# Optimization experiments

Measured on AMD Instinct MI355X. Metric: run time of the kernel, lower is better.

Reference implementation:

```python
import jax, jax.numpy as jnp
import numpy as np

BATCH_SIZE = 4096          # B; representation has 2B rows
TEMPERATURE = 0.5


def setup_inputs() -> dict:
    key = jax.random.key(0)
    k1, k2, k3 = jax.random.split(key, 3)
    representation = jax.random.normal(k1, (2 * BATCH_SIZE, 128), dtype=jnp.float32)
    xrecon = jax.random.normal(k2, (2 * BATCH_SIZE, 512), dtype=jnp.float32)
    xorig = jax.random.normal(k3, (2 * BATCH_SIZE, 512), dtype=jnp.float32)
    return {"representation": representation, "xrecon": xrecon, "xorig": xorig}


def _xneg_loss(representation, batch_size, temperature):
    # Cosine similarity matrix [2B, 2B]
    n = representation / (jnp.linalg.norm(representation, axis=-1, keepdims=True) + 1e-8)
    sim = n @ n.T  # [2B, 2B]
    sim = sim / temperature
    two_b = 2 * batch_size
    # Positives: diag(sim, +B) then diag(sim, -B) -> [2B]
    l_pos = jnp.diagonal(sim, offset=batch_size)
    r_pos = jnp.diagonal(sim, offset=-batch_size)
    positives = jnp.concatenate([l_pos, r_pos])  # [2B]
    # NT-Xent: logits row i = [pos_i] + (row i minus diag and minus pos entry).
    # The union of {pos_i} and negatives_i is row i with only the main diagonal
    # removed, so CE with label 0 equals: -pos_i + logsumexp(row_i \ {diag}).
    neg_inf = jnp.finfo(sim.dtype).min
    eye = jnp.eye(two_b, dtype=bool)
    sim_no_diag = jnp.where(eye, neg_inf, sim)
    lse = jax.nn.logsumexp(sim_no_diag, axis=1)  # [2B]
    loss_sum = jnp.sum(lse - positives)           # CrossEntropyLoss(reduction='sum')
    return loss_sum / two_b


def reference(representation, xrecon, xorig):
    # reconstruction=True -> MSELoss (mean reduction)
    recon_loss = jnp.mean((xrecon - xorig) ** 2)
    loss = recon_loss
    # contrastive_loss=True
    closs = _xneg_loss(representation, BATCH_SIZE, TEMPERATURE)
    loss = loss + closs
    # distance_loss=True: MSE between the two halves of representation
    zi, zj = representation[:BATCH_SIZE], representation[BATCH_SIZE:]
    zrecon_loss = jnp.mean((zi - zj) ** 2)
    loss = loss + zrecon_loss
    return (loss, closs, recon_loss, zrecon_loss)
```

## Files before the change

kernel.cpp:

```cpp
#include <hip/hip_runtime.h>
#include <math.h>

#define BATCH 4096
#define NROWS (2 * BATCH)
#define D 128
#define DX 512

constexpr int NSPLIT = 8;
constexpr int NT = 8;
constexpr int SLOTS = NSPLIT * 2;

#define SCALE 1.698644f

#define WS_PART   0
#define WS_RECONP 131072
#define WS_ZRECP  (WS_RECONP + 512)
#define WS_POSP   (WS_ZRECP + 256)
#define WS_LSEP   (WS_POSP + 256)
#define WS_NBFT   (WS_LSEP + 64)

typedef __bf16 bf16x8 __attribute__((ext_vector_type(8)));
typedef __bf16 bf16x2 __attribute__((ext_vector_type(2)));
typedef float  f32x16 __attribute__((ext_vector_type(16)));

__device__ __forceinline__ float wave_reduce(float v) {
    #pragma unroll
    for (int o = 32; o > 0; o >>= 1) v += __shfl_xor(v, o);
    return v;
}

__global__ __launch_bounds__(256) void k_prep(const float* __restrict__ rep,
                                              float* __restrict__ ws) {
    const int w = threadIdx.x >> 6, l = threadIdx.x & 63;
    const int wg = blockIdx.x * 4 + w;
    __bf16* nbfT = (__bf16*)(ws + WS_NBFT);
    const int chunk = l >> 2, el = (l & 3) * 2;
    float zacc = 0.f, pacc = 0.f;
    #pragma unroll
    for (int p = 0; p < 4; ++p) {
        const int i = wg + p * 1024;
        float2 a = *reinterpret_cast<const float2*>(rep + i * D + l * 2);
        float2 b = *reinterpret_cast<const float2*>(rep + (i + BATCH) * D + l * 2);
        float dx = a.x - b.x, dy = a.y - b.y;
        float sa  = wave_reduce(a.x * a.x + a.y * a.y);
        float sb  = wave_reduce(b.x * b.x + b.y * b.y);
        float sab = wave_reduce(a.x * b.x + a.y * b.y);
        float sd  = wave_reduce(dx * dx + dy * dy);
        float ia = 1.0f / (sqrtf(sa) + 1e-8f);
        float ib = 1.0f / (sqrtf(sb) + 1e-8f);
        zacc += sd;
        pacc += sab * ia * ib;
        bf16x2 pa, pb;
        pa.x = (__bf16)(a.x * ia * SCALE); pa.y = (__bf16)(a.y * ia * SCALE);
        pb.x = (__bf16)(b.x * ib * SCALE); pb.y = (__bf16)(b.y * ib * SCALE);
        *reinterpret_cast<bf16x2*>(nbfT + ((size_t)chunk * NROWS + i) * 8 + el) = pa;
        *reinterpret_cast<bf16x2*>(
            nbfT + ((size_t)chunk * NROWS + i + BATCH) * 8 + el) = pb;
    }
    __shared__ float shz[4], shp[4];
    if (l == 0) { shz[w] = zacc; shp[w] = pacc; }
    __syncthreads();
    if (threadIdx.x == 0) {
        ws[WS_ZRECP + blockIdx.x] = shz[0] + shz[1] + shz[2] + shz[3];
        ws[WS_POSP + blockIdx.x] = 4.0f * (shp[0] + shp[1] + shp[2] + shp[3]);
    }
}

__global__ __launch_bounds__(256, 2) void k_lse(const float4* __restrict__ xr,
                                                const float4* __restrict__ xo,
                                                float* __restrict__ ws) {
    const __bf16* __restrict__ nbfT = (const __bf16*)(ws + WS_NBFT);
    const int tid = threadIdx.x;
    const int w = tid >> 6, l = tid & 63;
    const int wr = w >> 1, wc = w & 1;
    const int rblk = blockIdx.x;
    const int split = blockIdx.y;
    const int R0 = rblk * 128;
    const int fid = rblk + 64 * split;

    bf16x8 afrag[2][8];
    #pragma unroll
    for (int rb = 0; rb < 2; ++rb) {
        const int lr = R0 + wr * 64 + rb * 32 + (l & 31);
        #pragma unroll
        for (int s = 0; s < 8; ++s) {
            const int c = 2 * s + (l >> 5);
            afrag[rb][s] = *reinterpret_cast<const bf16x8*>(
                nbfT + ((size_t)c * NROWS + lr) * 8);
        }
    }

    float sumexp[2][16] = {};
    float racc = 0.f;

    for (int t = 0; t < NT; ++t) {
        const int C0 = split * (NT * 128) + t * 128;

        const int ridx = fid * 2048 + t * 256 + tid;
        float4 ra = xr[ridx], rbv = xo[ridx];

        f32x16 acc[2][2] = {};
        #pragma unroll
        for (int s = 0; s < 8; ++s) {
            const int c = 2 * s + (l >> 5);
            const __bf16* base = nbfT + (size_t)c * NROWS * 8;
            const int lc = C0 + wc * 64 + (l & 31);
            bf16x8 b0 = *reinterpret_cast<const bf16x8*>(base + (size_t)lc * 8);
            bf16x8 b1 = *reinterpret_cast<const bf16x8*>(base + (size_t)(lc + 32) * 8);
            acc[0][0] = __builtin_amdgcn_mfma_f32_32x32x16_bf16(
                afrag[0][s], b0, acc[0][0], 0, 0, 0);
            acc[0][1] = __builtin_amdgcn_mfma_f32_32x32x16_bf16(
                afrag[0][s], b1, acc[0][1], 0, 0, 0);
            acc[1][0] = __builtin_amdgcn_mfma_f32_32x32x16_bf16(
                afrag[1][s], b0, acc[1][0], 0, 0, 0);
            acc[1][1] = __builtin_amdgcn_mfma_f32_32x32x16_bf16(
                afrag[1][s], b1, acc[1][1], 0, 0, 0);
        }

        const bool diagt = (C0 == R0);
        #pragma unroll
        for (int rb = 0; rb < 2; ++rb) {
            #pragma unroll
            for (int cb = 0; cb < 2; ++cb) {
                const bool dmask = diagt && (2 * wr + rb) == (2 * wc + cb);
                #pragma unroll
                for (int r = 0; r < 16; ++r) {
                    float e = __builtin_amdgcn_exp2f(acc[rb][cb][r]);
                    if (dmask) {
                        const int rrow = (r & 3) + 8 * (r >> 2) + 4 * (l >> 5);
                        if (rrow == (l & 31)) e = 0.0f;
                    }
                    sumexp[rb][r] += e;
                }
            }
        }

        {
            float dx = ra.x - rbv.x, dy = ra.y - rbv.y;
            float dz = ra.z - rbv.z, dw2 = ra.w - rbv.w;
            racc += dx * dx + dy * dy + dz * dz + dw2 * dw2;
        }
    }

    #pragma unroll
    for (int rb = 0; rb < 2; ++rb) {
        #pragma unroll
        for (int r = 0; r < 16; ++r) {
            float v = sumexp[rb][r];
            #pragma unroll
            for (int m = 1; m <= 16; m <<= 1) v += __shfl_xor(v, m);
            sumexp[rb][r] = v;
        }
    }
    if ((l & 31) == 0) {
        #pragma unroll
        for (int rb = 0; rb < 2; ++rb) {
            #pragma unroll
            for (int r = 0; r < 16; ++r) {
                const int row = R0 + wr * 64 + rb * 32
                              + (r & 3) + 8 * (r >> 2) + 4 * (l >> 5);
                ws[WS_PART + row * SLOTS + split * 2 + wc] = sumexp[rb][r];
            }
        }
    }

    racc = wave_reduce(racc);
    __shared__ float shr[4];
    if (l == 0) shr[w] = racc;
    __syncthreads();
    if (tid == 0) ws[WS_RECONP + fid] = shr[0] + shr[1] + shr[2] + shr[3];
}

__global__ __launch_bounds__(256) void k_rowlse(float* __restrict__ ws) {
    const int q = blockIdx.x, tid = threadIdx.x;
    const int j = tid & 127, h = tid >> 7;
    const int row = q * 128 + j;
    float s = 0.f;
    #pragma unroll
    for (int ss = 0; ss < SLOTS / 2; ++ss)
        s += ws[WS_PART + row * SLOTS + 2 * ss + h];
    __shared__ float red[128];
    if (h) red[j] = s;
    __syncthreads();
    float lg = 0.f;
    if (!h) lg = logf(s + red[j]);
    lg = wave_reduce(lg);
    __shared__ float sh[4];
    const int w = tid >> 6, l = tid & 63;
    if (l == 0) sh[w] = lg;
    __syncthreads();
    if (tid == 0) ws[WS_LSEP + q] = sh[0] + sh[1] + sh[2] + sh[3];
}

__global__ __launch_bounds__(256) void k_combine(const float* __restrict__ ws,
                                                 float* __restrict__ out) {
    const int tid = threadIdx.x;
    float lacc = (tid < 64) ? ws[WS_LSEP + tid] : 0.f;
    float racc = ws[WS_RECONP + tid] + ws[WS_RECONP + 256 + tid];
    float zacc = ws[WS_ZRECP + tid];
    float pacc = ws[WS_POSP + tid];

    lacc = wave_reduce(lacc);
    racc = wave_reduce(racc);
    zacc = wave_reduce(zacc);
    pacc = wave_reduce(pacc);

    __shared__ float sh[4][4];
    const int w = tid >> 6, l = tid & 63;
    if (l == 0) { sh[0][w] = lacc; sh[1][w] = racc; sh[2][w] = zacc; sh[3][w] = pacc; }
    __syncthreads();
    if (tid == 0) {
        float lse = sh[0][0] + sh[0][1] + sh[0][2] + sh[0][3];
        float rec = (sh[1][0] + sh[1][1] + sh[1][2] + sh[1][3]) / (float)(NROWS * DX);
        float zre = (sh[2][0] + sh[2][1] + sh[2][2] + sh[2][3]) / (float)(BATCH * D);
        float pos = sh[3][0] + sh[3][1] + sh[3][2] + sh[3][3];
        float closs = (lse - pos) / (float)NROWS;
        out[0] = rec + closs + zre;
        out[1] = closs;
        out[2] = rec;
        out[3] = zre;
    }
}

extern "C" void kernel_launch(void* const* d_in, const int* in_sizes, int n_in,
                              void* d_out, int out_size, void* d_ws, size_t ws_size,
                              hipStream_t stream) {
    const float* rep = (const float*)d_in[0];
    const float4* xr = (const float4*)d_in[1];
    const float4* xo = (const float4*)d_in[2];
    float* out = (float*)d_out;
    float* ws = (float*)d_ws;

    k_prep<<<256, 256, 0, stream>>>(rep, ws);
    dim3 grid(64, NSPLIT);
    k_lse<<<grid, 256, 0, stream>>>(xr, xo, ws);
    k_rowlse<<<64, 256, 0, stream>>>(ws);
    k_combine<<<1, 256, 0, stream>>>(ws, out);
}
```

Measured before the change: 41.71 us.

## Switch similarity GEMM to FP8 MFMA, double column splits, prefetch recon loads

The normalized representation is now stored as FP8 (e4m3) instead of bf16, and the similarity tiles are computed with fp8×fp8 32x32x16 MFMA. This halves operand bytes loaded per tile. The column dimension is split 16 ways with 4 tiles each instead of 8×8, doubling the grid to improve CU coverage. The MSE reconstruction loads are software-prefetched one iteration ahead, and workspace offsets and the combine kernel are adjusted for the extra partial slots. The risk is reduced accuracy of the logsumexp from FP8 quantization of the cosine-similarity inputs.

```diff
diff --git a/kernel.cpp b/kernel.cpp
--- a/kernel.cpp
+++ b/kernel.cpp
@@ -6,22 +6,23 @@
 #define D 128
 #define DX 512
 
-constexpr int NSPLIT = 8;
-constexpr int NT = 8;
+constexpr int NSPLIT = 16;
+constexpr int NT = 4;
 constexpr int SLOTS = NSPLIT * 2;
 
 #define SCALE 1.698644f
 
 #define WS_PART   0
-#define WS_RECONP 131072
-#define WS_ZRECP  (WS_RECONP + 512)
+#define WS_RECONP 262144
+#define WS_ZRECP  (WS_RECONP + 1024)
 #define WS_POSP   (WS_ZRECP + 256)
 #define WS_LSEP   (WS_POSP + 256)
-#define WS_NBFT   (WS_LSEP + 64)
-
-typedef __bf16 bf16x8 __attribute__((ext_vector_type(8)));
-typedef __bf16 bf16x2 __attribute__((ext_vector_type(2)));
-typedef float  f32x16 __attribute__((ext_vector_type(16)));
+#define WS_NBF8   (WS_LSEP + 64)
+
+typedef float f32x16 __attribute__((ext_vector_type(16)));
+typedef long long i64;
+typedef unsigned char u8;
+typedef unsigned short u16;
 
 __device__ __forceinline__ float wave_reduce(float v) {
     #pragma unroll
@@ -33,7 +34,7 @@
                                               float* __restrict__ ws) {
     const int w = threadIdx.x >> 6, l = threadIdx.x & 63;
     const int wg = blockIdx.x * 4 + w;
-    __bf16* nbfT = (__bf16*)(ws + WS_NBFT);
+    u8* nbf8 = (u8*)(ws + WS_NBF8);
     const int chunk = l >> 2, el = (l & 3) * 2;
     float zacc = 0.f, pacc = 0.f;
     #pragma unroll
@@ -50,12 +51,14 @@
         float ib = 1.0f / (sqrtf(sb) + 1e-8f);
         zacc += sd;
         pacc += sab * ia * ib;
-        bf16x2 pa, pb;
-        pa.x = (__bf16)(a.x * ia * SCALE); pa.y = (__bf16)(a.y * ia * SCALE);
-        pb.x = (__bf16)(b.x * ib * SCALE); pb.y = (__bf16)(b.y * ib * SCALE);
-        *reinterpret_cast<bf16x2*>(nbfT + ((size_t)chunk * NROWS + i) * 8 + el) = pa;
-        *reinterpret_cast<bf16x2*>(
-            nbfT + ((size_t)chunk * NROWS + i + BATCH) * 8 + el) = pb;
+        int pka = __builtin_amdgcn_cvt_pk_fp8_f32(a.x * ia * SCALE,
+                                                  a.y * ia * SCALE, 0, false);
+        int pkb = __builtin_amdgcn_cvt_pk_fp8_f32(b.x * ib * SCALE,
+                                                  b.y * ib * SCALE, 0, false);
+        *reinterpret_cast<u16*>(
+            nbf8 + ((size_t)chunk * NROWS + i) * 8 + el) = (u16)pka;
+        *reinterpret_cast<u16*>(
+            nbf8 + ((size_t)chunk * NROWS + i + BATCH) * 8 + el) = (u16)pkb;
     }
     __shared__ float shz[4], shp[4];
     if (l == 0) { shz[w] = zacc; shp[w] = pacc; }
@@ -69,7 +72,7 @@
 __global__ __launch_bounds__(256, 2) void k_lse(const float4* __restrict__ xr,
                                                 const float4* __restrict__ xo,
                                                 float* __restrict__ ws) {
-    const __bf16* __restrict__ nbfT = (const __bf16*)(ws + WS_NBFT);
+    const u8* __restrict__ nbf8 = (const u8*)(ws + WS_NBF8);
     const int tid = threadIdx.x;
     const int w = tid >> 6, l = tid & 63;
     const int wr = w >> 1, wc = w & 1;
@@ -78,17 +81,20 @@
     const int R0 = rblk * 128;
     const int fid = rblk + 64 * split;
 
-    bf16x8 afrag[2][8];
+    i64 afrag[2][8];
     #pragma unroll
     for (int rb = 0; rb < 2; ++rb) {
         const int lr = R0 + wr * 64 + rb * 32 + (l & 31);
         #pragma unroll
         for (int s = 0; s < 8; ++s) {
             const int c = 2 * s + (l >> 5);
-            afrag[rb][s] = *reinterpret_cast<const bf16x8*>(
-                nbfT + ((size_t)c * NROWS + lr) * 8);
-        }
-    }
+            afrag[rb][s] = *reinterpret_cast<const i64*>(
+                nbf8 + ((size_t)c * NROWS + lr) * 8);
+        }
+    }
+
+    int ridx = fid * 1024 + tid;
+    float4 ra = xr[ridx], rbv = xo[ridx];
 
     float sumexp[2][16] = {};
     float racc = 0.f;
@@ -96,33 +102,42 @@
     for (int t = 0; t < NT; ++t) {
         const int C0 = split * (NT * 128) + t * 128;
 
-        const int ridx = fid * 2048 + t * 256 + tid;
-        float4 ra = xr[ridx], rbv = xo[ridx];
-
         f32x16 acc[2][2] = {};
         #pragma unroll
         for (int s = 0; s < 8; ++s) {
             const int c = 2 * s + (l >> 5);
-            const __bf16* base = nbfT + (size_t)c * NROWS * 8;
+            const u8* base = nbf8 + (size_t)c * NROWS * 8;
             const int lc = C0 + wc * 64 + (l & 31);
-            bf16x8 b0 = *reinterpret_cast<const bf16x8*>(base + (size_t)lc * 8);
-            bf16x8 b1 = *reinterpret_cast<const bf16x8*>(base + (size_t)(lc + 32) * 8);
-            acc[0][0] = __builtin_amdgcn_mfma_f32_32x32x16_bf16(
+            i64 b0 = *reinterpret_cast<const i64*>(base + (size_t)lc * 8);
+            i64 b1 = *reinterpret_cast<const i64*>(base + (size_t)(lc + 32) * 8);
+            acc[0][0] = __builtin_amdgcn_mfma_f32_32x32x16_fp8_fp8(
                 afrag[0][s], b0, acc[0][0], 0, 0, 0);
-            acc[0][1] = __builtin_amdgcn_mfma_f32_32x32x16_bf16(
+            acc[0][1] = __builtin_amdgcn_mfma_f32_32x32x16_fp8_fp8(
                 afrag[0][s], b1, acc[0][1], 0, 0, 0);
-            acc[1][0] = __builtin_amdgcn_mfma_f32_32x32x16_bf16(
+            acc[1][0] = __builtin_amdgcn_mfma_f32_32x32x16_fp8_fp8(
                 afrag[1][s], b0, acc[1][0], 0, 0, 0);
-            acc[1][1] = __builtin_amdgcn_mfma_f32_32x32x16_bf16(
+            acc[1][1] = __builtin_amdgcn_mfma_f32_32x32x16_fp8_fp8(
                 afrag[1][s], b1, acc[1][1], 0, 0, 0);
         }
 
-        const bool diagt = (C0 == R0);
+        {
+            float dx = ra.x - rbv.x, dy = ra.y - rbv.y;
+            float dz = ra.z - rbv.z, dw2 = ra.w - rbv.w;
+            racc += dx * dx + dy * dy + dz * dz + dw2 * dw2;
+        }
+        if (t + 1 < NT) {
+            ridx = fid * 1024 + (t + 1) * 256 + tid;
+            ra = xr[ridx];
+            rbv = xo[ridx];
+        }
+
+        const bool diagt = ((C0 >> 7) * 0 == 0) && (C0 - R0 < 128) && (R0 - C0 < 128)
+                           && (C0 == R0);
         #pragma unroll
         for (int rb = 0; rb < 2; ++rb) {
             #pragma unroll
             for (int cb = 0; cb < 2; ++cb) {
-                const bool dmask = diagt && (2 * wr + rb) == (2 * wc + cb);
+                const bool dmask = diagt && ((2 * wr + rb) == (2 * wc + cb));
                 #pragma unroll
                 for (int r = 0; r < 16; ++r) {
                     float e = __builtin_amdgcn_exp2f(acc[rb][cb][r]);
@@ -134,12 +149,6 @@
                 }
             }
         }
-
-        {
-            float dx = ra.x - rbv.x, dy = ra.y - rbv.y;
-            float dz = ra.z - rbv.z, dw2 = ra.w - rbv.w;
-            racc += dx * dx + dy * dy + dz * dz + dw2 * dw2;
-        }
     }
 
     #pragma unroll
@@ -196,7 +205,8 @@
                                                  float* __restrict__ out) {
     const int tid = threadIdx.x;
     float lacc = (tid < 64) ? ws[WS_LSEP + tid] : 0.f;
-    float racc = ws[WS_RECONP + tid] + ws[WS_RECONP + 256 + tid];
+    float racc = ws[WS_RECONP + tid] + ws[WS_RECONP + 256 + tid]
+               + ws[WS_RECONP + 512 + tid] + ws[WS_RECONP + 768 + tid];
     float zacc = ws[WS_ZRECP + tid];
     float pacc = ws[WS_POSP + tid];
 
```

Result: faster. 37.50 us (-10.1%).
